# Optimization experiments

Hardware: AMD Instinct MI355X
Metric: run time of the kernel (lower is better)

The kernel has to match this reference:

```python
import jax, jax.numpy as jnp
import numpy as np

N, IN_C, OUT_C, H = 100000, 256, 64, 8
K_CURV = 1.0      # manifold curvature k (Lorentz: t = sqrt(||s||^2 + k))
POWER_K = 2.0     # power_k of fp feature map


def fp(x, p):
    # norm(x) / (norm(x**p) + eps) * x**p, norms over last dim
    eps = 1e-12
    xp = x ** p
    norm_x = jnp.linalg.norm(x, axis=-1, keepdims=True)
    norm_xp = jnp.linalg.norm(xp, axis=-1, keepdims=True)
    return norm_x / (norm_xp + eps) * xp


def setup_inputs() -> dict:
    key = jax.random.key(0)
    ks = jax.random.split(key, 8)
    s = 1.0 / np.sqrt(IN_C)
    sm = 1.0 / np.sqrt(OUT_C)
    return {
        "query_input": jax.random.normal(ks[0], (N, IN_C), jnp.float32),
        # per-head HypLinear weights (stacked over heads)
        "Wq": jax.random.uniform(ks[1], (H, IN_C, OUT_C), jnp.float32, -s, s),
        "bq": jnp.zeros((H, OUT_C), jnp.float32),
        "Wk": jax.random.uniform(ks[2], (H, IN_C, OUT_C), jnp.float32, -s, s),
        "bk": jnp.zeros((H, OUT_C), jnp.float32),
        "Wv": jax.random.uniform(ks[3], (H, IN_C, OUT_C), jnp.float32, -s, s),
        "bv": jnp.zeros((H, OUT_C), jnp.float32),
        "norm_scale": jnp.ones((), jnp.float32),
        # v_map_mlp: Linear(out_channels, out_channels)
        "Wm": jax.random.uniform(ks[4], (OUT_C, OUT_C), jnp.float32, -sm, sm),
        "bm": jnp.zeros((OUT_C,), jnp.float32),
    }


def reference(query_input, Wq, bq, Wk, bk, Wv, bv, norm_scale, Wm, bm):
    # HypLinear per head: space part = x @ W + b; the time part
    # sqrt(||space||^2 + k) is dropped by [..., 1:] in linear_focus_attention,
    # so only the space components are computed.  shapes: [N, H, OUT_C]
    qs = jnp.einsum('nd,hdo->nho', query_input, Wq) + bq
    ks_ = jnp.einsum('nd,hdo->nho', query_input, Wk) + bk
    v = jnp.einsum('nd,hdo->nho', query_input, Wv) + bv

    denom_s = jnp.abs(norm_scale) + 1e-6
    phi_q = fp((jax.nn.relu(qs) + 1e-6) / denom_s, POWER_K)
    phi_k = fp((jax.nn.relu(ks_) + 1e-6) / denom_s, POWER_K)

    # linear attention: O(N * H * m * d)
    kT_v = jnp.einsum('nhm,nhd->hmd', phi_k, v)          # [H, m, d]
    numerator = jnp.einsum('nhm,hmd->nhd', phi_q, kT_v)  # [N, H, d]
    sum_k = phi_k.sum(axis=0)                            # [H, m]
    denominator = jnp.einsum('nhd,hd->nh', phi_q, sum_k)[..., None]
    attn = numerator / (denominator + 1e-6)

    # residual v-map MLP
    attn = attn + (jnp.einsum('nhd,de->nhe', v, Wm) + bm)

    # trans_heads_concat=False -> mean over heads
    out = attn.mean(axis=1)                              # [N, OUT_C]

    # lift back to Lorentz: prepend time component
    t = jnp.sqrt((out ** 2).sum(axis=-1, keepdims=True) + K_CURV)
    return jnp.concatenate([t, out], axis=-1)            # [N, OUT_C+1]
```

## Files before the change

kernel.cpp:

```cpp
#include <hip/hip_runtime.h>
#include <hip/hip_bf16.h>

#define NROWS 100000
#define NH 8
#define RPC 1568
#define NSUB 49
#define K2CH 98

typedef short s16x8 __attribute__((ext_vector_type(8)));
typedef float f32x4 __attribute__((ext_vector_type(4)));
typedef unsigned short u16;

__device__ __forceinline__ u16 f2bf(float f) {
  union { float f; unsigned u; } x; x.f = f;
  unsigned r = (x.u + 0x7FFFu + ((x.u >> 16) & 1u)) >> 16;
  return (u16)r;
}
__device__ __forceinline__ float bf2f(u16 b) {
  union { unsigned u; float f; } x; x.u = ((unsigned)b) << 16;
  return x.f;
}
__device__ __forceinline__ unsigned cvt2bf(float lo, float hi) {
  unsigned r;
  asm("v_cvt_pk_bf16_f32 %0, %1, %2" : "=v"(r) : "v"(lo), "v"(hi));
  return r;
}
__device__ __forceinline__ ushort4 cvt4bf(float a, float b, float c, float d) {
  union { unsigned u[2]; ushort4 s; } r;
  r.u[0] = cvt2bf(a, b);
  r.u[1] = cvt2bf(c, d);
  return r.s;
}

__device__ __forceinline__ void wg_barrier_lds() {
  asm volatile("s_waitcnt lgkmcnt(0)" ::: "memory");
  __builtin_amdgcn_s_barrier();
  asm volatile("" ::: "memory");
}

__global__ __launch_bounds__(256) void k0_pack(
    const float* __restrict__ Wq, const float* __restrict__ Wk,
    const float* __restrict__ Wv, u16* __restrict__ Wp)
{
  int t = blockIdx.x * 256 + threadIdx.x;
  int lane = t & 63;
  int rest = t >> 6;
  int s = rest % 48;
  int hc = rest / 48;
  int c2 = hc & 1, h = hc >> 1;
  int ml = lane & 15, sgk = lane >> 4;
  const float* W; int col, ks;
  if (s < 32) { int tl = s >> 3; ks = s & 7; W = c2 ? Wk : Wq; col = tl * 16 + ml; }
  else        { int tv = (s >> 3) - 4; ks = s & 7; W = Wv; col = c2 * 32 + tv * 16 + ml; }
  int k0 = ks * 32 + sgk * 8;
  u16 o[8];
#pragma unroll
  for (int j = 0; j < 8; j++)
    o[j] = f2bf(W[((size_t)h * 256 + k0 + j) * 64 + col]);
  ushort4* dst = (ushort4*)(Wp + (size_t)t * 8);
  dst[0] = make_ushort4(o[0], o[1], o[2], o[3]);
  dst[1] = make_ushort4(o[4], o[5], o[6], o[7]);
}

__global__ __launch_bounds__(256, 2) void k1_gemm_phi(
    const float* __restrict__ x, const u16* __restrict__ Wp,
    const float* __restrict__ bq, const float* __restrict__ bk,
    const float* __restrict__ bv, const float* __restrict__ nsc,
    u16* __restrict__ phi_q, u16* __restrict__ phi_k, u16* __restrict__ vout)
{
  __shared__ u16 xs[32 * 256];
  __shared__ u16 vws[32 * 64 * 8];
  __shared__ u16 stq[4 * 16 * 72];
  __shared__ u16 stv[32 * 72];
  __shared__ float biasl[192];

  const int tid = threadIdx.x;
  const int wv = tid >> 6, lane = tid & 63;
  const int c2 = wv & 1, rg = wv >> 1;
  const int m = lane & 15, sg = lane >> 4;
  const int rc = blockIdx.x & 63, h = blockIdx.x >> 6;
  const int n0 = rc * RPC;

  if (tid < 192) {
    const float* bp = tid < 64 ? bq : (tid < 128 ? bk : bv);
    biasl[tid] = bp[h * 64 + (tid & 63)];
  }

  const u16* wb = Wp + (size_t)(h * 2 + c2) * (48 * 64 * 8);
  s16x8 wq[4][8];
#pragma unroll
  for (int t = 0; t < 4; t++)
#pragma unroll
    for (int ks = 0; ks < 8; ks++)
      wq[t][ks] = *(const s16x8*)(wb + ((t * 8 + ks) * 64 + lane) * 8);

#pragma unroll
  for (int i2 = 0; i2 < 8; i2++) {
    int u = tid + i2 * 256;
    int tl = u >> 9, ks = (u >> 6) & 7, ln = u & 63;
    const u16* src = Wp + ((size_t)(h * 2 + (tl >> 1)) * 48 + 32 + (tl & 1) * 8 + ks) * (64 * 8)
                     + (size_t)ln * 8;
    *(s16x8*)(vws + (size_t)u * 8) = *(const s16x8*)src;
  }

#pragma unroll
  for (int i = 0; i < 4; i++) {
    int cu = tid + i * 256;
    int row = cu >> 5, c = cu & 31;
    int n = n0 + row; if (n >= NROWS) n = NROWS - 1;
    const float* src = x + (size_t)n * 256 + c * 8;
    float4 f0 = *(const float4*)src;
    float4 f1 = *(const float4*)(src + 4);
    union { unsigned u[4]; s16x8 v; } pk;
    pk.u[0] = cvt2bf(f0.x, f0.y);
    pk.u[1] = cvt2bf(f0.z, f0.w);
    pk.u[2] = cvt2bf(f1.x, f1.y);
    pk.u[3] = cvt2bf(f1.z, f1.w);
    *(s16x8*)(xs + row * 256 + ((c ^ (row & 7)) * 8)) = pk.v;
  }
  __syncthreads();

  const float inv_denom = 1.0f / (fabsf(nsc[0]) + 1e-6f);
  u16* const xbase = xs + (rg * 16 + m) * 256;
  const int sw = m & 7;

  for (int s = 0; s < NSUB; s++) {
    float4 xl[8];
    if (s + 1 < NSUB) {
      int nb = n0 + (s + 1) * 32;
#pragma unroll
      for (int i = 0; i < 4; i++) {
        int cu = tid + i * 256;
        int row = cu >> 5, c = cu & 31;
        int n = nb + row; if (n >= NROWS) n = NROWS - 1;
        const float* src = x + (size_t)n * 256 + c * 8;
        xl[i * 2]     = *(const float4*)src;
        xl[i * 2 + 1] = *(const float4*)(src + 4);
      }
    }

    f32x4 aq[4], av[2];
#pragma unroll
    for (int t = 0; t < 4; t++) aq[t] = (f32x4){0.f, 0.f, 0.f, 0.f};
    av[0] = (f32x4){0.f, 0.f, 0.f, 0.f};
    av[1] = (f32x4){0.f, 0.f, 0.f, 0.f};
#pragma unroll
    for (int ks = 0; ks < 8; ks++) {
      s16x8 bf = *(const s16x8*)(xbase + (((ks * 4 + sg) ^ sw) * 8));
#pragma unroll
      for (int t = 0; t < 4; t++)
        aq[t] = __builtin_amdgcn_mfma_f32_16x16x32_bf16(wq[t][ks], bf, aq[t], 0, 0, 0);
      s16x8 vw0 = *(const s16x8*)(vws + (((c2 * 2 + 0) * 8 + ks) * 64 + lane) * 8);
      s16x8 vw1 = *(const s16x8*)(vws + (((c2 * 2 + 1) * 8 + ks) * 64 + lane) * 8);
      av[0] = __builtin_amdgcn_mfma_f32_16x16x32_bf16(vw0, bf, av[0], 0, 0, 0);
      av[1] = __builtin_amdgcn_mfma_f32_16x16x32_bf16(vw1, bf, av[1], 0, 0, 0);
    }

    f32x4 bqk[4], bvv[2];
#pragma unroll
    for (int t = 0; t < 4; t++) bqk[t] = *(const f32x4*)&biasl[c2 * 64 + t * 16 + sg * 4];
#pragma unroll
    for (int tv = 0; tv < 2; tv++) bvv[tv] = *(const f32x4*)&biasl[128 + c2 * 32 + tv * 16 + sg * 4];

    float vq[4][4];
    float s2 = 0.f, s4 = 0.f;
#pragma unroll
    for (int t = 0; t < 4; t++)
#pragma unroll
      for (int r = 0; r < 4; r++) {
        float y = (fmaxf(aq[t][r] + bqk[t][r], 0.f) + 1e-6f) * inv_denom;
        float y2 = y * y;
        vq[t][r] = y2;
        s2 += y2; s4 += y2 * y2;
      }
    s2 += __shfl_xor(s2, 16); s2 += __shfl_xor(s2, 32);
    s4 += __shfl_xor(s4, 16); s4 += __shfl_xor(s4, 32);
    float sc = sqrtf(s2) / (sqrtf(s4) + 1e-12f);

    {
      u16* sq = stq + wv * 1152 + m * 72;
#pragma unroll
      for (int t = 0; t < 4; t++)
        *(ushort4*)(sq + ((t + m) & 3) * 16 + sg * 4) =
          cvt4bf(vq[t][0] * sc, vq[t][1] * sc, vq[t][2] * sc, vq[t][3] * sc);
      int rowl = rg * 16 + m;
      u16* sv = stv + rowl * 72;
#pragma unroll
      for (int tv = 0; tv < 2; tv++) {
        int tc = c2 * 2 + tv;
        f32x4 a = av[tv], b = bvv[tv];
        *(ushort4*)(sv + ((tc + rowl) & 3) * 16 + sg * 4) =
          cvt4bf(a[0] + b[0], a[1] + b[1], a[2] + b[2], a[3] + b[3]);
      }
    }
    {
      int r_ = lane >> 2, tc = lane & 3;
      const u16* a = stq + wv * 1152 + r_ * 72 + ((tc + r_) & 3) * 16;
      s16x8 p0 = *(const s16x8*)a;
      s16x8 p1 = *(const s16x8*)(a + 8);
      int n = n0 + s * 32 + rg * 16 + r_;
      if (n < NROWS) {
        u16* dst = (c2 ? phi_k : phi_q) + ((size_t)h * NROWS + n) * 64 + tc * 16;
        *(s16x8*)dst = p0;
        *(s16x8*)(dst + 8) = p1;
      }
    }
    wg_barrier_lds();

    {
      int row = wv * 8 + (lane >> 3);
      int hc8 = lane & 7, tc = hc8 >> 1, half = hc8 & 1;
      const u16* a = stv + row * 72 + ((tc + row) & 3) * 16 + half * 8;
      s16x8 pv = *(const s16x8*)a;
      int n = n0 + s * 32 + row;
      if (n < NROWS)
        *(s16x8*)(vout + ((size_t)h * NROWS + n) * 64 + tc * 16 + half * 8) = pv;
    }
    if (s + 1 < NSUB) {
#pragma unroll
      for (int i = 0; i < 4; i++) {
        int cu = tid + i * 256;
        int row = cu >> 5, c = cu & 31;
        float4 f0 = xl[i * 2], f1 = xl[i * 2 + 1];
        union { unsigned u[4]; s16x8 v; } pk;
        pk.u[0] = cvt2bf(f0.x, f0.y);
        pk.u[1] = cvt2bf(f0.z, f0.w);
        pk.u[2] = cvt2bf(f1.x, f1.y);
        pk.u[3] = cvt2bf(f1.z, f1.w);
        *(s16x8*)(xs + row * 256 + ((c ^ (row & 7)) * 8)) = pk.v;
      }
    }
    wg_barrier_lds();
  }
}

__global__ __launch_bounds__(256) void k2_ktv(
    const u16* __restrict__ phi_k, const u16* __restrict__ vin,
    float* __restrict__ P)
{
  __shared__ u16 pkT[2][64][72];
  __shared__ u16 vT[2][64][72];
  const int tid = threadIdx.x;
  const int h = blockIdx.y;
  const int r0 = blockIdx.x * 1024;
  const int wv = tid >> 6, lane = tid & 63;
  const int m = lane & 15, sg = lane >> 4;
  const int c4 = (tid & 15) * 4, rgp = tid >> 4;

  const u16* pkb = phi_k + (size_t)h * (NROWS * 64);
  const u16* vb  = vin  + (size_t)h * (NROWS * 64);

  f32x4 acc[4];
#pragma unroll
  for (int t = 0; t < 4; t++) acc[t] = (f32x4){0.f, 0.f, 0.f, 0.f};
  f32x4 accs = (f32x4){0.f, 0.f, 0.f, 0.f};
  s16x8 onesf;
#pragma unroll
  for (int j = 0; j < 8; j++) onesf[j] = (m == 0) ? (short)0x3F80 : (short)0;

  ushort4 pk4[4], vv4[4];
#define K2_LOAD(sub)                                                        \
  {                                                                         \
    int nb = r0 + (sub) * 64 + rgp * 4;                                     \
    _Pragma("unroll")                                                       \
    for (int i = 0; i < 4; i++) {                                           \
      int n = nb + i;                                                       \
      if (n < NROWS) {                                                      \
        pk4[i] = *(const ushort4*)(pkb + (size_t)n * 64 + c4);              \
        vv4[i] = *(const ushort4*)(vb  + (size_t)n * 64 + c4);              \
      } else {                                                              \
        pk4[i] = make_ushort4(0, 0, 0, 0);                                  \
        vv4[i] = make_ushort4(0, 0, 0, 0);                                  \
      }                                                                     \
    }                                                                       \
  }
#define K2_WRITE(buf)                                                       \
  {                                                                         \
    *(ushort4*)&pkT[buf][c4 + 0][rgp * 4] = make_ushort4(pk4[0].x, pk4[1].x, pk4[2].x, pk4[3].x); \
    *(ushort4*)&pkT[buf][c4 + 1][rgp * 4] = make_ushort4(pk4[0].y, pk4[1].y, pk4[2].y, pk4[3].y); \
    *(ushort4*)&pkT[buf][c4 + 2][rgp * 4] = make_ushort4(pk4[0].z, pk4[1].z, pk4[2].z, pk4[3].z); \
    *(ushort4*)&pkT[buf][c4 + 3][rgp * 4] = make_ushort4(pk4[0].w, pk4[1].w, pk4[2].w, pk4[3].w); \
    *(ushort4*)&vT[buf][c4 + 0][rgp * 4]  = make_ushort4(vv4[0].x, vv4[1].x, vv4[2].x, vv4[3].x); \
    *(ushort4*)&vT[buf][c4 + 1][rgp * 4]  = make_ushort4(vv4[0].y, vv4[1].y, vv4[2].y, vv4[3].y); \
    *(ushort4*)&vT[buf][c4 + 2][rgp * 4]  = make_ushort4(vv4[0].z, vv4[1].z, vv4[2].z, vv4[3].z); \
    *(ushort4*)&vT[buf][c4 + 3][rgp * 4]  = make_ushort4(vv4[0].w, vv4[1].w, vv4[2].w, vv4[3].w); \
  }

  K2_LOAD(0); K2_WRITE(0);
  __syncthreads();

  for (int sub = 0; sub < 16; sub++) {
    int cur = sub & 1;
    if (sub + 1 < 16) K2_LOAD(sub + 1);
#pragma unroll
    for (int ks = 0; ks < 2; ks++) {
      s16x8 af = *(const s16x8*)&pkT[cur][wv * 16 + m][ks * 32 + sg * 8];
#pragma unroll
      for (int t = 0; t < 4; t++) {
        s16x8 bfv = *(const s16x8*)&vT[cur][t * 16 + m][ks * 32 + sg * 8];
        acc[t] = __builtin_amdgcn_mfma_f32_16x16x32_bf16(af, bfv, acc[t], 0, 0, 0);
      }
      accs = __builtin_amdgcn_mfma_f32_16x16x32_bf16(af, onesf, accs, 0, 0, 0);
    }
    if (sub + 1 < 16) K2_WRITE(cur ^ 1);
    __syncthreads();
  }

  float* pb = P + (size_t)(blockIdx.x * NH + h) * (65 * 64);
  int mm = wv * 16 + sg * 4;
#pragma unroll
  for (int t = 0; t < 4; t++)
#pragma unroll
    for (int r = 0; r < 4; r++)
      pb[(t * 16 + m) * 64 + mm + r] = acc[t][r];
  if (m == 0)
#pragma unroll
    for (int r = 0; r < 4; r++)
      pb[64 * 64 + mm + r] = accs[r];
}

__global__ __launch_bounds__(256) void k25_pack(
    const float* __restrict__ P, const float* __restrict__ Wm,
    u16* __restrict__ kTvT, u16* __restrict__ WmP)
{
  int idx = blockIdx.x * 256 + threadIdx.x;
  if (idx < NH * 65 * 64) {
    float s = 0.f;
    for (int rcc = 0; rcc < K2CH; rcc++)
      s += P[(size_t)rcc * (NH * 65 * 64) + idx];
    kTvT[idx] = f2bf(s);
  } else if (idx < NH * 65 * 64 + 64 * 64) {
    int j = idx - NH * 65 * 64;
    WmP[j] = f2bf(Wm[(j & 63) * 64 + (j >> 6)]);
  }
}

__global__ __launch_bounds__(512, 2) void k3_out(
    const u16* __restrict__ phi_q, const u16* __restrict__ vin,
    const u16* __restrict__ kTvT, const u16* __restrict__ WmP,
    const float* __restrict__ bm, float* __restrict__ out)
{
  __shared__ u16 kbl[37376];

  const int tid = threadIdx.x;
  const int wv = tid >> 6, lane = tid & 63;
  const int m = lane & 15, sg = lane >> 4;
  const int n0 = blockIdx.x * 128;
  const int rw = wv * 16;
  const int n = n0 + rw + m;

  for (int i = tid; i < 4672; i += 512) {
    int e0 = i * 8;
    s16x8 val = *(const s16x8*)(kTvT + e0);
    int r = e0 >> 6;
    *(s16x8*)&kbl[e0 ^ ((r & 7) << 3)] = val;
  }
  __syncthreads();

#define KBL_FRAG(rowlin, off) \
  (*(const s16x8*)&kbl[(((rowlin) * 64 + (off)) ^ (((rowlin) & 7) << 3))])

  f32x4 zero4 = {0.f, 0.f, 0.f, 0.f};
  s16x8 zero8 = {0, 0, 0, 0, 0, 0, 0, 0};
  f32x4 osum[4];
#pragma unroll
  for (int t = 0; t < 4; t++) osum[t] = zero4;

  float va[2][8];
#pragma unroll
  for (int ks = 0; ks < 2; ks++)
#pragma unroll
    for (int j = 0; j < 8; j++) va[ks][j] = 0.f;

  s16x8 aqn[2];
#pragma unroll
  for (int ks = 0; ks < 2; ks++)
    aqn[ks] = *(const s16x8*)(phi_q + (size_t)n * 64 + ks * 32 + sg * 8);

  for (int h = 0; h < NH; h++) {
    s16x8 aq0 = aqn[0], aq1 = aqn[1];
    s16x8 v80 = *(const s16x8*)(vin + (size_t)h * (NROWS * 64) + (size_t)n * 64 + sg * 8);
    s16x8 v81 = *(const s16x8*)(vin + (size_t)h * (NROWS * 64) + (size_t)n * 64 + 32 + sg * 8);
    if (h + 1 < NH) {
      const u16* pq = phi_q + (size_t)(h + 1) * (NROWS * 64) + (size_t)n * 64;
      aqn[0] = *(const s16x8*)(pq + sg * 8);
      aqn[1] = *(const s16x8*)(pq + 32 + sg * 8);
    }

    const int rl = h * 65;
    f32x4 accn[4];
#pragma unroll
    for (int t = 0; t < 4; t++) accn[t] = zero4;
    f32x4 accd = zero4;
    {
#pragma unroll
      for (int t = 0; t < 4; t++) {
        s16x8 bfv = KBL_FRAG(rl + t * 16 + m, sg * 8);
        accn[t] = __builtin_amdgcn_mfma_f32_16x16x32_bf16(aq0, bfv, accn[t], 0, 0, 0);
      }
      s16x8 bd = zero8;
      if (m == 0) bd = KBL_FRAG(rl + 64, sg * 8);
      accd = __builtin_amdgcn_mfma_f32_16x16x32_bf16(aq0, bd, accd, 0, 0, 0);
    }
    {
#pragma unroll
      for (int t = 0; t < 4; t++) {
        s16x8 bfv = KBL_FRAG(rl + t * 16 + m, 32 + sg * 8);
        accn[t] = __builtin_amdgcn_mfma_f32_16x16x32_bf16(aq1, bfv, accn[t], 0, 0, 0);
      }
      s16x8 bd = zero8;
      if (m == 0) bd = KBL_FRAG(rl + 64, 32 + sg * 8);
      accd = __builtin_amdgcn_mfma_f32_16x16x32_bf16(aq1, bd, accd, 0, 0, 0);
    }

#pragma unroll
    for (int j = 0; j < 8; j++) va[0][j] += bf2f((u16)v80[j]);
#pragma unroll
    for (int j = 0; j < 8; j++) va[1][j] += bf2f((u16)v81[j]);

#pragma unroll
    for (int r = 0; r < 4; r++) {
      float den = __shfl(accd[r], lane & 48);
      float rinv = 1.0f / (den + 1e-6f);
#pragma unroll
      for (int t = 0; t < 4; t++) osum[t][r] += accn[t][r] * rinv;
    }
  }

  s16x8 vbf[2];
#pragma unroll
  for (int ks = 0; ks < 2; ks++) {
    union { unsigned u[4]; s16x8 v; } pk;
#pragma unroll
    for (int j = 0; j < 4; j++)
      pk.u[j] = cvt2bf(va[ks][2 * j] * 0.125f, va[ks][2 * j + 1] * 0.125f);
    vbf[ks] = pk.v;
  }

  f32x4 accr[4];
#pragma unroll
  for (int t = 0; t < 4; t++) accr[t] = zero4;
#pragma unroll
  for (int ks = 0; ks < 2; ks++)
#pragma unroll
    for (int t = 0; t < 4; t++) {
      s16x8 bw = KBL_FRAG(520 + t * 16 + m, ks * 32 + sg * 8);
      accr[t] = __builtin_amdgcn_mfma_f32_16x16x32_bf16(vbf[ks], bw, accr[t], 0, 0, 0);
    }

  float bmv[4];
#pragma unroll
  for (int t = 0; t < 4; t++) bmv[t] = bm[t * 16 + m];

#pragma unroll
  for (int r = 0; r < 4; r++) {
    int nn = n0 + rw + sg * 4 + r;
    float v4[4];
    float ssq = 0.f;
#pragma unroll
    for (int t = 0; t < 4; t++) {
      float o = osum[t][r] * 0.125f + accr[t][r] + bmv[t];
      v4[t] = o;
      ssq += o * o;
    }
    ssq += __shfl_xor(ssq, 1);
    ssq += __shfl_xor(ssq, 2);
    ssq += __shfl_xor(ssq, 4);
    ssq += __shfl_xor(ssq, 8);
    if (nn < NROWS) {
      if (m == 0) out[(size_t)nn * 65] = sqrtf(ssq + 1.0f);
#pragma unroll
      for (int t = 0; t < 4; t++)
        out[(size_t)nn * 65 + 1 + t * 16 + m] = v4[t];
    }
  }
}

extern "C" void kernel_launch(void* const* d_in, const int* in_sizes, int n_in,
                              void* d_out, int out_size, void* d_ws, size_t ws_size,
                              hipStream_t stream) {
  const float* x   = (const float*)d_in[0];
  const float* Wq  = (const float*)d_in[1];
  const float* bq  = (const float*)d_in[2];
  const float* Wk  = (const float*)d_in[3];
  const float* bk  = (const float*)d_in[4];
  const float* Wv  = (const float*)d_in[5];
  const float* bv  = (const float*)d_in[6];
  const float* nsc = (const float*)d_in[7];
  const float* Wm  = (const float*)d_in[8];
  const float* bm  = (const float*)d_in[9];
  float* out = (float*)d_out;

  char* ws = (char*)d_ws;
  const size_t PHI_BYTES = (size_t)NROWS * NH * 64 * 2;
  u16* phi_q = (u16*)(ws);
  u16* phi_k = (u16*)(ws + PHI_BYTES);
  u16* vv    = (u16*)(ws + 2 * PHI_BYTES);
  u16* Wp    = (u16*)(ws + 3 * PHI_BYTES);
  char* p    = ws + 3 * PHI_BYTES + 786432;
  float* P   = (float*)(p);
  u16* kTvT  = (u16*)(p + 13066240);
  u16* WmP   = (u16*)(p + 13066240 + 66560);

  k0_pack<<<192, 256, 0, stream>>>(Wq, Wk, Wv, Wp);
  k1_gemm_phi<<<512, 256, 0, stream>>>(x, Wp, bq, bk, bv, nsc, phi_q, phi_k, vv);
  dim3 g2(K2CH, NH);
  k2_ktv<<<g2, 256, 0, stream>>>(phi_k, vv, P);
  k25_pack<<<(NH * 65 * 64 + 64 * 64 + 255) / 256, 256, 0, stream>>>(P, Wm, kTvT, WmP);
  k3_out<<<(NROWS + 127) / 128, 512, 0, stream>>>(phi_q, vv, kTvT, WmP, bm, out);
}
```

Measured before the change: 397.5 us.

## Fuse phi_k^T V reduction into the projection kernel, drop phi_k buffer

The separate k2_ktv kernel is removed. Each k1 block now accumulates phi_k^T·v and the column sums of phi_k with MFMA straight from double-buffered LDS staging tiles, one sub-tile behind the projection. It writes per-chunk partials to P, and the final reduction runs over 64 chunks instead of 98. This avoids writing and re-reading the 12.8MB phi_k array and saves a kernel launch, at the cost of more LDS, scalar-gathered LDS operand loads, and extra MFMA work inside the main GEMM loop.

```diff
diff --git a/kernel.cpp b/kernel.cpp
--- a/kernel.cpp
+++ b/kernel.cpp
@@ -5,7 +5,7 @@
 #define NH 8
 #define RPC 1568
 #define NSUB 49
-#define K2CH 98
+#define NCH1 64
 
 typedef short s16x8 __attribute__((ext_vector_type(8)));
 typedef float f32x4 __attribute__((ext_vector_type(4)));
@@ -66,12 +66,12 @@
     const float* __restrict__ x, const u16* __restrict__ Wp,
     const float* __restrict__ bq, const float* __restrict__ bk,
     const float* __restrict__ bv, const float* __restrict__ nsc,
-    u16* __restrict__ phi_q, u16* __restrict__ phi_k, u16* __restrict__ vout)
+    u16* __restrict__ phi_q, u16* __restrict__ vout, float* __restrict__ P)
 {
   __shared__ u16 xs[32 * 256];
   __shared__ u16 vws[32 * 64 * 8];
-  __shared__ u16 stq[4 * 16 * 72];
-  __shared__ u16 stv[32 * 72];
+  __shared__ u16 stq[2][4 * 16 * 72];
+  __shared__ u16 stv[2][32 * 72];
   __shared__ float biasl[192];
 
   const int tid = threadIdx.x;
@@ -124,7 +124,41 @@
   u16* const xbase = xs + (rg * 16 + m) * 256;
   const int sw = m & 7;
 
+  f32x4 kacc[4];
+#pragma unroll
+  for (int t = 0; t < 4; t++) kacc[t] = (f32x4){0.f, 0.f, 0.f, 0.f};
+  f32x4 ksum = (f32x4){0.f, 0.f, 0.f, 0.f};
+  s16x8 onesf;
+#pragma unroll
+  for (int j = 0; j < 8; j++) onesf[j] = (m == 0) ? (short)0x3F80 : (short)0;
+
+#define KTV_ACC(pbuf)                                                        \
+  {                                                                          \
+    const u16* sqs = stq[pbuf] + ((sg < 2) ? 1 : 3) * 1152;                  \
+    const u16* svb = stv[pbuf];                                              \
+    short afe[8];                                                            \
+    _Pragma("unroll")                                                        \
+    for (int j = 0; j < 8; j++) {                                            \
+      int rl = (sg * 8 + j) & 15;                                            \
+      afe[j] = (short)sqs[rl * 72 + (((wv + rl) & 3) << 4) + m];             \
+    }                                                                        \
+    s16x8 af = {afe[0], afe[1], afe[2], afe[3], afe[4], afe[5], afe[6], afe[7]}; \
+    _Pragma("unroll")                                                        \
+    for (int dcb = 0; dcb < 4; dcb++) {                                      \
+      short be[8];                                                           \
+      _Pragma("unroll")                                                      \
+      for (int j = 0; j < 8; j++) {                                          \
+        int row = sg * 8 + j;                                                \
+        be[j] = (short)svb[row * 72 + (((dcb + row) & 3) << 4) + m];         \
+      }                                                                      \
+      s16x8 bv8 = {be[0], be[1], be[2], be[3], be[4], be[5], be[6], be[7]};  \
+      kacc[dcb] = __builtin_amdgcn_mfma_f32_16x16x32_bf16(af, bv8, kacc[dcb], 0, 0, 0); \
+    }                                                                        \
+    ksum = __builtin_amdgcn_mfma_f32_16x16x32_bf16(af, onesf, ksum, 0, 0, 0); \
+  }
+
   for (int s = 0; s < NSUB; s++) {
+    const int buf = s & 1;
     float4 xl[8];
     if (s + 1 < NSUB) {
       int nb = n0 + (s + 1) * 32;
@@ -139,6 +173,8 @@
       }
     }
 
+    if (s > 0 && n0 + (s - 1) * 32 < NROWS) KTV_ACC(buf ^ 1);
+
     f32x4 aq[4], av[2];
 #pragma unroll
     for (int t = 0; t < 4; t++) aq[t] = (f32x4){0.f, 0.f, 0.f, 0.f};
@@ -178,13 +214,13 @@
     float sc = sqrtf(s2) / (sqrtf(s4) + 1e-12f);
 
     {
-      u16* sq = stq + wv * 1152 + m * 72;
+      u16* sq = stq[buf] + wv * 1152 + m * 72;
 #pragma unroll
       for (int t = 0; t < 4; t++)
         *(ushort4*)(sq + ((t + m) & 3) * 16 + sg * 4) =
           cvt4bf(vq[t][0] * sc, vq[t][1] * sc, vq[t][2] * sc, vq[t][3] * sc);
       int rowl = rg * 16 + m;
-      u16* sv = stv + rowl * 72;
+      u16* sv = stv[buf] + rowl * 72;
 #pragma unroll
       for (int tv = 0; tv < 2; tv++) {
         int tc = c2 * 2 + tv;
@@ -193,14 +229,14 @@
           cvt4bf(a[0] + b[0], a[1] + b[1], a[2] + b[2], a[3] + b[3]);
       }
     }
-    {
+    if (!c2) {
       int r_ = lane >> 2, tc = lane & 3;
-      const u16* a = stq + wv * 1152 + r_ * 72 + ((tc + r_) & 3) * 16;
+      const u16* a = stq[buf] + wv * 1152 + r_ * 72 + ((tc + r_) & 3) * 16;
       s16x8 p0 = *(const s16x8*)a;
       s16x8 p1 = *(const s16x8*)(a + 8);
       int n = n0 + s * 32 + rg * 16 + r_;
       if (n < NROWS) {
-        u16* dst = (c2 ? phi_k : phi_q) + ((size_t)h * NROWS + n) * 64 + tc * 16;
+        u16* dst = phi_q + ((size_t)h * NROWS + n) * 64 + tc * 16;
         *(s16x8*)dst = p0;
         *(s16x8*)(dst + 8) = p1;
       }
@@ -210,7 +246,7 @@
     {
       int row = wv * 8 + (lane >> 3);
       int hc8 = lane & 7, tc = hc8 >> 1, half = hc8 & 1;
-      const u16* a = stv + row * 72 + ((tc + row) & 3) * 16 + half * 8;
+      const u16* a = stv[buf] + row * 72 + ((tc + row) & 3) * 16 + half * 8;
       s16x8 pv = *(const s16x8*)a;
       int n = n0 + s * 32 + row;
       if (n < NROWS)
@@ -232,91 +268,22 @@
     }
     wg_barrier_lds();
   }
-}
-
-__global__ __launch_bounds__(256) void k2_ktv(
-    const u16* __restrict__ phi_k, const u16* __restrict__ vin,
-    float* __restrict__ P)
-{
-  __shared__ u16 pkT[2][64][72];
-  __shared__ u16 vT[2][64][72];
-  const int tid = threadIdx.x;
-  const int h = blockIdx.y;
-  const int r0 = blockIdx.x * 1024;
-  const int wv = tid >> 6, lane = tid & 63;
-  const int m = lane & 15, sg = lane >> 4;
-  const int c4 = (tid & 15) * 4, rgp = tid >> 4;
-
-  const u16* pkb = phi_k + (size_t)h * (NROWS * 64);
-  const u16* vb  = vin  + (size_t)h * (NROWS * 64);
-
-  f32x4 acc[4];
-#pragma unroll
-  for (int t = 0; t < 4; t++) acc[t] = (f32x4){0.f, 0.f, 0.f, 0.f};
-  f32x4 accs = (f32x4){0.f, 0.f, 0.f, 0.f};
-  s16x8 onesf;
-#pragma unroll
-  for (int j = 0; j < 8; j++) onesf[j] = (m == 0) ? (short)0x3F80 : (short)0;
-
-  ushort4 pk4[4], vv4[4];
-#define K2_LOAD(sub)                                                        \
-  {                                                                         \
-    int nb = r0 + (sub) * 64 + rgp * 4;                                     \
-    _Pragma("unroll")                                                       \
-    for (int i = 0; i < 4; i++) {                                           \
-      int n = nb + i;                                                       \
-      if (n < NROWS) {                                                      \
-        pk4[i] = *(const ushort4*)(pkb + (size_t)n * 64 + c4);              \
-        vv4[i] = *(const ushort4*)(vb  + (size_t)n * 64 + c4);              \
-      } else {                                                              \
-        pk4[i] = make_ushort4(0, 0, 0, 0);                                  \
-        vv4[i] = make_ushort4(0, 0, 0, 0);                                  \
-      }                                                                     \
-    }                                                                       \
-  }
-#define K2_WRITE(buf)                                                       \
-  {                                                                         \
-    *(ushort4*)&pkT[buf][c4 + 0][rgp * 4] = make_ushort4(pk4[0].x, pk4[1].x, pk4[2].x, pk4[3].x); \
-    *(ushort4*)&pkT[buf][c4 + 1][rgp * 4] = make_ushort4(pk4[0].y, pk4[1].y, pk4[2].y, pk4[3].y); \
-    *(ushort4*)&pkT[buf][c4 + 2][rgp * 4] = make_ushort4(pk4[0].z, pk4[1].z, pk4[2].z, pk4[3].z); \
-    *(ushort4*)&pkT[buf][c4 + 3][rgp * 4] = make_ushort4(pk4[0].w, pk4[1].w, pk4[2].w, pk4[3].w); \
-    *(ushort4*)&vT[buf][c4 + 0][rgp * 4]  = make_ushort4(vv4[0].x, vv4[1].x, vv4[2].x, vv4[3].x); \
-    *(ushort4*)&vT[buf][c4 + 1][rgp * 4]  = make_ushort4(vv4[0].y, vv4[1].y, vv4[2].y, vv4[3].y); \
-    *(ushort4*)&vT[buf][c4 + 2][rgp * 4]  = make_ushort4(vv4[0].z, vv4[1].z, vv4[2].z, vv4[3].z); \
-    *(ushort4*)&vT[buf][c4 + 3][rgp * 4]  = make_ushort4(vv4[0].w, vv4[1].w, vv4[2].w, vv4[3].w); \
-  }
-
-  K2_LOAD(0); K2_WRITE(0);
-  __syncthreads();
-
-  for (int sub = 0; sub < 16; sub++) {
-    int cur = sub & 1;
-    if (sub + 1 < 16) K2_LOAD(sub + 1);
-#pragma unroll
-    for (int ks = 0; ks < 2; ks++) {
-      s16x8 af = *(const s16x8*)&pkT[cur][wv * 16 + m][ks * 32 + sg * 8];
-#pragma unroll
-      for (int t = 0; t < 4; t++) {
-        s16x8 bfv = *(const s16x8*)&vT[cur][t * 16 + m][ks * 32 + sg * 8];
-        acc[t] = __builtin_amdgcn_mfma_f32_16x16x32_bf16(af, bfv, acc[t], 0, 0, 0);
-      }
-      accs = __builtin_amdgcn_mfma_f32_16x16x32_bf16(af, onesf, accs, 0, 0, 0);
-    }
-    if (sub + 1 < 16) K2_WRITE(cur ^ 1);
-    __syncthreads();
-  }
-
-  float* pb = P + (size_t)(blockIdx.x * NH + h) * (65 * 64);
-  int mm = wv * 16 + sg * 4;
-#pragma unroll
-  for (int t = 0; t < 4; t++)
-#pragma unroll
-    for (int r = 0; r < 4; r++)
-      pb[(t * 16 + m) * 64 + mm + r] = acc[t][r];
-  if (m == 0)
-#pragma unroll
-    for (int r = 0; r < 4; r++)
-      pb[64 * 64 + mm + r] = accs[r];
+
+  if (n0 + (NSUB - 1) * 32 < NROWS) KTV_ACC((NSUB - 1) & 1);
+
+  {
+    float* pb = P + (size_t)(rc * NH + h) * (65 * 64);
+    int mm = wv * 16 + sg * 4;
+#pragma unroll
+    for (int dcb = 0; dcb < 4; dcb++)
+#pragma unroll
+      for (int r = 0; r < 4; r++)
+        pb[(dcb * 16 + m) * 64 + mm + r] = kacc[dcb][r];
+    if (m == 0)
+#pragma unroll
+      for (int r = 0; r < 4; r++)
+        pb[64 * 64 + mm + r] = ksum[r];
+  }
 }
 
 __global__ __launch_bounds__(256) void k25_pack(
@@ -326,7 +293,7 @@
   int idx = blockIdx.x * 256 + threadIdx.x;
   if (idx < NH * 65 * 64) {
     float s = 0.f;
-    for (int rcc = 0; rcc < K2CH; rcc++)
+    for (int rcc = 0; rcc < NCH1; rcc++)
       s += P[(size_t)rcc * (NH * 65 * 64) + idx];
     kTvT[idx] = f2bf(s);
   } else if (idx < NH * 65 * 64 + 64 * 64) {
@@ -494,18 +461,15 @@
   char* ws = (char*)d_ws;
   const size_t PHI_BYTES = (size_t)NROWS * NH * 64 * 2;
   u16* phi_q = (u16*)(ws);
-  u16* phi_k = (u16*)(ws + PHI_BYTES);
-  u16* vv    = (u16*)(ws + 2 * PHI_BYTES);
-  u16* Wp    = (u16*)(ws + 3 * PHI_BYTES);
-  char* p    = ws + 3 * PHI_BYTES + 786432;
+  u16* vv    = (u16*)(ws + PHI_BYTES);
+  u16* Wp    = (u16*)(ws + 2 * PHI_BYTES);
+  char* p    = ws + 2 * PHI_BYTES + 786432;
   float* P   = (float*)(p);
-  u16* kTvT  = (u16*)(p + 13066240);
-  u16* WmP   = (u16*)(p + 13066240 + 66560);
+  u16* kTvT  = (u16*)(p + 8519680);
+  u16* WmP   = (u16*)(p + 8519680 + 66560);
 
   k0_pack<<<192, 256, 0, stream>>>(Wq, Wk, Wv, Wp);
-  k1_gemm_phi<<<512, 256, 0, stream>>>(x, Wp, bq, bk, bv, nsc, phi_q, phi_k, vv);
-  dim3 g2(K2CH, NH);
-  k2_ktv<<<g2, 256, 0, stream>>>(phi_k, vv, P);
+  k1_gemm_phi<<<512, 256, 0, stream>>>(x, Wp, bq, bk, bv, nsc, phi_q, vv, P);
   k25_pack<<<(NH * 65 * 64 + 64 * 64 + 255) / 256, 256, 0, stream>>>(P, Wm, kTvT, WmP);
   k3_out<<<(NROWS + 127) / 128, 512, 0, stream>>>(phi_q, vv, kTvT, WmP, bm, out);
 }
```

Result: slower. 542.3 us (+36.5%).

## Swizzle k2 LDS transpose layout and deepen register prefetch pipeline

Applied to the files above, without the earlier changes.

In the kT·v reduction kernel, the LDS column index is now XOR-swizzled on write and read to cut bank conflicts in the transposed stores and MFMA fragment reads. The loop is restructured with two register staging sets, so global loads for sub-tile s+2 and s+3 are issued two steps ahead. The loop is manually unrolled by two with lighter LDS-only barriers. This costs more registers and relies on the swizzle staying consistent between writes and reads.

```diff
diff --git a/kernel.cpp b/kernel.cpp
--- a/kernel.cpp
+++ b/kernel.cpp
@@ -245,7 +245,10 @@
   const int r0 = blockIdx.x * 1024;
   const int wv = tid >> 6, lane = tid & 63;
   const int m = lane & 15, sg = lane >> 4;
-  const int c4 = (tid & 15) * 4, rgp = tid >> 4;
+  const int t15 = tid & 15, rgp = tid >> 4;
+  const int c4 = t15 * 4;
+  const int wsw = (rgp * 4) ^ ((t15 & 3) << 3);
+  const int rsw = (m >> 2) << 3;
 
   const u16* pkb = phi_k + (size_t)h * (NROWS * 64);
   const u16* vb  = vin  + (size_t)h * (NROWS * 64);
@@ -258,52 +261,64 @@
 #pragma unroll
   for (int j = 0; j < 8; j++) onesf[j] = (m == 0) ? (short)0x3F80 : (short)0;
 
-  ushort4 pk4[4], vv4[4];
-#define K2_LOAD(sub)                                                        \
+  ushort4 pkA[4], vvA[4], pkB[4], vvB[4];
+
+#define K2_LOAD(dP, dV, sub)                                                \
   {                                                                         \
     int nb = r0 + (sub) * 64 + rgp * 4;                                     \
     _Pragma("unroll")                                                       \
     for (int i = 0; i < 4; i++) {                                           \
       int n = nb + i;                                                       \
       if (n < NROWS) {                                                      \
-        pk4[i] = *(const ushort4*)(pkb + (size_t)n * 64 + c4);              \
-        vv4[i] = *(const ushort4*)(vb  + (size_t)n * 64 + c4);              \
+        dP[i] = *(const ushort4*)(pkb + (size_t)n * 64 + c4);               \
+        dV[i] = *(const ushort4*)(vb  + (size_t)n * 64 + c4);               \
       } else {                                                              \
-        pk4[i] = make_ushort4(0, 0, 0, 0);                                  \
-        vv4[i] = make_ushort4(0, 0, 0, 0);                                  \
+        dP[i] = make_ushort4(0, 0, 0, 0);                                   \
+        dV[i] = make_ushort4(0, 0, 0, 0);                                   \
       }                                                                     \
     }                                                                       \
   }
-#define K2_WRITE(buf)                                                       \
+#define K2_WRITE(buf, sP, sV)                                               \
   {                                                                         \
-    *(ushort4*)&pkT[buf][c4 + 0][rgp * 4] = make_ushort4(pk4[0].x, pk4[1].x, pk4[2].x, pk4[3].x); \
-    *(ushort4*)&pkT[buf][c4 + 1][rgp * 4] = make_ushort4(pk4[0].y, pk4[1].y, pk4[2].y, pk4[3].y); \
-    *(ushort4*)&pkT[buf][c4 + 2][rgp * 4] = make_ushort4(pk4[0].z, pk4[1].z, pk4[2].z, pk4[3].z); \
-    *(ushort4*)&pkT[buf][c4 + 3][rgp * 4] = make_ushort4(pk4[0].w, pk4[1].w, pk4[2].w, pk4[3].w); \
-    *(ushort4*)&vT[buf][c4 + 0][rgp * 4]  = make_ushort4(vv4[0].x, vv4[1].x, vv4[2].x, vv4[3].x); \
-    *(ushort4*)&vT[buf][c4 + 1][rgp * 4]  = make_ushort4(vv4[0].y, vv4[1].y, vv4[2].y, vv4[3].y); \
-    *(ushort4*)&vT[buf][c4 + 2][rgp * 4]  = make_ushort4(vv4[0].z, vv4[1].z, vv4[2].z, vv4[3].z); \
-    *(ushort4*)&vT[buf][c4 + 3][rgp * 4]  = make_ushort4(vv4[0].w, vv4[1].w, vv4[2].w, vv4[3].w); \
-  }
-
-  K2_LOAD(0); K2_WRITE(0);
-  __syncthreads();
-
-  for (int sub = 0; sub < 16; sub++) {
-    int cur = sub & 1;
-    if (sub + 1 < 16) K2_LOAD(sub + 1);
-#pragma unroll
-    for (int ks = 0; ks < 2; ks++) {
-      s16x8 af = *(const s16x8*)&pkT[cur][wv * 16 + m][ks * 32 + sg * 8];
-#pragma unroll
-      for (int t = 0; t < 4; t++) {
-        s16x8 bfv = *(const s16x8*)&vT[cur][t * 16 + m][ks * 32 + sg * 8];
-        acc[t] = __builtin_amdgcn_mfma_f32_16x16x32_bf16(af, bfv, acc[t], 0, 0, 0);
-      }
-      accs = __builtin_amdgcn_mfma_f32_16x16x32_bf16(af, onesf, accs, 0, 0, 0);
-    }
-    if (sub + 1 < 16) K2_WRITE(cur ^ 1);
-    __syncthreads();
+    *(ushort4*)&pkT[buf][c4 + 0][wsw] = make_ushort4(sP[0].x, sP[1].x, sP[2].x, sP[3].x); \
+    *(ushort4*)&pkT[buf][c4 + 1][wsw] = make_ushort4(sP[0].y, sP[1].y, sP[2].y, sP[3].y); \
+    *(ushort4*)&pkT[buf][c4 + 2][wsw] = make_ushort4(sP[0].z, sP[1].z, sP[2].z, sP[3].z); \
+    *(ushort4*)&pkT[buf][c4 + 3][wsw] = make_ushort4(sP[0].w, sP[1].w, sP[2].w, sP[3].w); \
+    *(ushort4*)&vT[buf][c4 + 0][wsw]  = make_ushort4(sV[0].x, sV[1].x, sV[2].x, sV[3].x); \
+    *(ushort4*)&vT[buf][c4 + 1][wsw]  = make_ushort4(sV[0].y, sV[1].y, sV[2].y, sV[3].y); \
+    *(ushort4*)&vT[buf][c4 + 2][wsw]  = make_ushort4(sV[0].z, sV[1].z, sV[2].z, sV[3].z); \
+    *(ushort4*)&vT[buf][c4 + 3][wsw]  = make_ushort4(sV[0].w, sV[1].w, sV[2].w, sV[3].w); \
+  }
+#define K2_MFMA(buf)                                                        \
+  {                                                                         \
+    _Pragma("unroll")                                                       \
+    for (int ks = 0; ks < 2; ks++) {                                        \
+      s16x8 af = *(const s16x8*)&pkT[buf][wv * 16 + m][(ks * 32 + sg * 8) ^ rsw]; \
+      _Pragma("unroll")                                                     \
+      for (int t = 0; t < 4; t++) {                                         \
+        s16x8 bfv = *(const s16x8*)&vT[buf][t * 16 + m][(ks * 32 + sg * 8) ^ rsw]; \
+        acc[t] = __builtin_amdgcn_mfma_f32_16x16x32_bf16(af, bfv, acc[t], 0, 0, 0); \
+      }                                                                     \
+      accs = __builtin_amdgcn_mfma_f32_16x16x32_bf16(af, onesf, accs, 0, 0, 0); \
+    }                                                                       \
+  }
+
+  K2_LOAD(pkA, vvA, 0);
+  K2_WRITE(0, pkA, vvA);
+  K2_LOAD(pkB, vvB, 1);
+  wg_barrier_lds();
+
+#pragma unroll 1
+  for (int sp = 0; sp < 8; sp++) {
+    int s0 = sp * 2;
+    K2_MFMA(0);
+    K2_WRITE(1, pkB, vvB);
+    if (s0 + 2 < 16) K2_LOAD(pkA, vvA, s0 + 2);
+    wg_barrier_lds();
+    K2_MFMA(1);
+    if (s0 + 2 < 16) K2_WRITE(0, pkA, vvA);
+    if (s0 + 3 < 16) K2_LOAD(pkB, vvB, s0 + 3);
+    wg_barrier_lds();
   }
 
   float* pb = P + (size_t)(blockIdx.x * NH + h) * (65 * 64);
```

Result: no change. 392.5 us (-1.2%).
